# Kernel tuning notes

Measured on AMD Instinct MI355X. Metric: run time of the kernel, lower is better.

## Reference

```python
import jax, jax.numpy as jnp
import numpy as np

B, N, P = 8192, 4096, 8
D = N // P  # 512
EPS = 1e-5


def setup_inputs() -> dict:
    key = jax.random.key(0)
    ks = jax.random.split(key, 7)
    bound = 1.0 / np.sqrt(D)
    return {
        "x": jax.random.normal(ks[0], (B, N), dtype=jnp.float32),
        "weights1": jax.random.normal(ks[1], (P, D, D), dtype=jnp.float32) * bound,
        "bias1": jax.random.uniform(ks[2], (N,), jnp.float32, -bound, bound),
        "weights2": jax.random.normal(ks[3], (P, D, D), dtype=jnp.float32) * bound,
        "bias2": jax.random.uniform(ks[4], (N,), jnp.float32, -bound, bound),
        "bn_weight": jnp.ones((N,), jnp.float32),
        "bn_bias": jnp.zeros((N,), jnp.float32),
        "gamma3": jax.random.normal(ks[5], (N,), jnp.float32) * 0.1,
        "beta3": jax.random.normal(ks[6], (N,), jnp.float32) * 0.1,
    }


def _block_matmul(x, w):
    # x: [B, N], w: [P, D, D] -> equivalent to x @ block_diag(*w)
    b = x.shape[0]
    return jnp.einsum("bpd,pde->bpe", x.reshape(b, P, D), w).reshape(b, N)


def reference(x, weights1, bias1, weights2, bias2, bn_weight, bn_bias, gamma3, beta3):
    h = _block_matmul(x, weights1) + bias1  # [B, N]
    # BatchNorm1d in training mode: biased batch statistics over the batch axis
    mean = jnp.mean(h, axis=0)
    var = jnp.mean((h - mean) ** 2, axis=0)
    o1 = (h - mean) * jax.lax.rsqrt(var + EPS) * bn_weight + bn_bias
    o3 = _block_matmul(o1, weights2) + bias2 + x  # residual
    # sigmoid-gated activation: (gamma + sigmoid(beta*x)*(1-gamma)) * x
    o4 = (gamma3 + jax.nn.sigmoid(beta3 * o3) * (1.0 - gamma3)) * o3
    return o4
```

## Files before the change

### kernel.cpp

```cpp
#include <hip/hip_runtime.h>
#include <hip/hip_bf16.h>
#include <cstdint>
#include <cstddef>

#define B_ROWS 8192
#define N_COLS 4096
#define P_BLK 8
#define D_BLK 512
#define EPSV 1e-5f

typedef __bf16 bf16x8 __attribute__((ext_vector_type(8)));
typedef float f32x4 __attribute__((ext_vector_type(4)));

__device__ __forceinline__ void async_ld16(const void* g, void* l) {
    __builtin_amdgcn_global_load_lds(
        (const __attribute__((address_space(1))) void*)g,
        (__attribute__((address_space(3))) void*)l,
        16, 0, 0);
}

__device__ __forceinline__ void decode_tile(int n, int& row_base, int& col_base) {
    const int row_tile = n >> 5;
    const int col_tile = ((n & 7) << 2) | ((n >> 3) & 3);
    row_base = row_tile * 128;
    col_base = col_tile * 128;
}

__global__ __launch_bounds__(256) void cvt_x_k(const float* __restrict__ x,
                                               __hip_bfloat16* __restrict__ xb) {
    size_t i = ((size_t)blockIdx.x * 256 + threadIdx.x) * 8;
    float4 v0 = *(const float4*)(x + i);
    float4 v1 = *(const float4*)(x + i + 4);
    union { __hip_bfloat16 h[8]; uint4 u; } r;
    r.h[0] = __float2bfloat16(v0.x); r.h[1] = __float2bfloat16(v0.y);
    r.h[2] = __float2bfloat16(v0.z); r.h[3] = __float2bfloat16(v0.w);
    r.h[4] = __float2bfloat16(v1.x); r.h[5] = __float2bfloat16(v1.y);
    r.h[6] = __float2bfloat16(v1.z); r.h[7] = __float2bfloat16(v1.w);
    *(uint4*)(xb + i) = r.u;
}

__global__ __launch_bounds__(256) void tr_w_k(const float* __restrict__ W,
                                              const float* __restrict__ scale,
                                              __hip_bfloat16* __restrict__ Wt) {
    __shared__ float t[32][33];
    int p = blockIdx.z;
    int d0 = blockIdx.x * 32, e0 = blockIdx.y * 32;
    const float* Wp = W + (size_t)p * D_BLK * D_BLK;
    for (int j = 0; j < 32; j += 8) {
        int d = d0 + threadIdx.y + j;
        float v = Wp[(size_t)d * D_BLK + e0 + threadIdx.x];
        if (scale) v *= scale[p * D_BLK + d];
        t[threadIdx.y + j][threadIdx.x] = v;
    }
    __syncthreads();
    __hip_bfloat16* Wtp = Wt + (size_t)p * D_BLK * D_BLK;
    for (int j = 0; j < 32; j += 8) {
        int e = e0 + threadIdx.y + j;
        Wtp[(size_t)e * D_BLK + d0 + threadIdx.x] =
            __float2bfloat16(t[threadIdx.x][threadIdx.y + j]);
    }
}

__global__ __launch_bounds__(256) void finalize_k(const float* __restrict__ sum,
                                                  const float* __restrict__ sumsq,
                                                  const float* __restrict__ bnw,
                                                  const float* __restrict__ bnb,
                                                  float* __restrict__ a,
                                                  float* __restrict__ c) {
    int i = blockIdx.x * 256 + threadIdx.x;
    float m = sum[i] * (1.0f / B_ROWS);
    float var = sumsq[i] * (1.0f / B_ROWS) - m * m;
    float ai = bnw[i] * rsqrtf(var + EPSV);
    a[i] = ai;
    c[i] = bnb[i] - m * ai;
}

__global__ __launch_bounds__(256) void bias2p_k(const float* __restrict__ W2,
                                                const float* __restrict__ c,
                                                const float* __restrict__ bias2,
                                                float* __restrict__ out) {
    int col = blockIdx.x * 256 + threadIdx.x;
    int p = col >> 9;
    int e = col & (D_BLK - 1);
    int d0 = blockIdx.y * (D_BLK / 8);
    const float* Wp = W2 + (size_t)p * D_BLK * D_BLK + (size_t)d0 * D_BLK + e;
    const float* cp = c + p * D_BLK + d0;
    float acc = (blockIdx.y == 0) ? bias2[col] : 0.0f;
    for (int d = 0; d < D_BLK / 8; d++) acc += cp[d] * Wp[(size_t)d * D_BLK];
    atomicAdd(&out[col], acc);
}

__device__ __forceinline__ void gemm_core(const __hip_bfloat16* __restrict__ A,
                                          const __hip_bfloat16* __restrict__ Bt,
                                          int row_base, int col_base,
                                          f32x4 acc[4][4]) {
    __shared__ __hip_bfloat16 As[2][128 * 32];
    __shared__ __hip_bfloat16 Bs[2][128 * 32];

    const int tid = threadIdx.x;
    const int lane = tid & 63;
    const int wave = tid >> 6;
    const int wm = (wave >> 1) * 64;
    const int wn = (wave & 1) * 64;
    const int p = col_base >> 9;
    const int ebase = col_base & (D_BLK - 1);

    const int ar = tid >> 2;
    const int c4 = tid & 3;
    const int kq8 = (c4 ^ ((tid >> 3) & 3)) * 8;
    const int dst_off = ar * 32 + c4 * 8;

    const __hip_bfloat16* a_src0 = A + (size_t)(row_base + ar) * N_COLS + p * D_BLK + kq8;
    const __hip_bfloat16* a_src1 = a_src0 + (size_t)64 * N_COLS;
    const __hip_bfloat16* b_src0 = Bt + (size_t)(p * D_BLK + ebase + ar) * D_BLK + kq8;
    const __hip_bfloat16* b_src1 = b_src0 + (size_t)64 * D_BLK;

    const int fm = lane & 15;
    const int fkoff = ((lane >> 4) ^ ((fm >> 1) & 3)) * 8;

    for (int i = 0; i < 4; i++)
        for (int j = 0; j < 4; j++)
            acc[i][j] = (f32x4){0.0f, 0.0f, 0.0f, 0.0f};

    async_ld16(a_src0, &As[0][dst_off]);
    async_ld16(a_src1, &As[0][dst_off + 64 * 32]);
    async_ld16(b_src0, &Bs[0][dst_off]);
    async_ld16(b_src1, &Bs[0][dst_off + 64 * 32]);

    int cur = 0;
    for (int k0 = 0; k0 < D_BLK; k0 += 32) {
        if (k0 + 32 < D_BLK) {
            __hip_bfloat16* ad = &As[cur ^ 1][dst_off];
            __hip_bfloat16* bd = &Bs[cur ^ 1][dst_off];
            async_ld16(a_src0 + 32, ad);
            async_ld16(a_src1 + 32, ad + 64 * 32);
            async_ld16(b_src0 + 32, bd);
            async_ld16(b_src1 + 32, bd + 64 * 32);
            a_src0 += 32; a_src1 += 32; b_src0 += 32; b_src1 += 32;
            asm volatile("s_waitcnt vmcnt(4)" ::: "memory");
        } else {
            asm volatile("s_waitcnt vmcnt(0)" ::: "memory");
        }
        __builtin_amdgcn_s_barrier();
        asm volatile("" ::: "memory");

        bf16x8 af[4], bfr[4];
        const __hip_bfloat16* Asc = &As[cur][0];
        const __hip_bfloat16* Bsc = &Bs[cur][0];
#pragma unroll
        for (int i = 0; i < 4; i++)
            af[i] = *(const bf16x8*)&Asc[(wm + i * 16 + fm) * 32 + fkoff];
#pragma unroll
        for (int j = 0; j < 4; j++)
            bfr[j] = *(const bf16x8*)&Bsc[(wn + j * 16 + fm) * 32 + fkoff];
        asm volatile("s_waitcnt lgkmcnt(0)" ::: "memory");
        __builtin_amdgcn_sched_barrier(0);
        __builtin_amdgcn_s_barrier();
        asm volatile("" ::: "memory");

#pragma unroll
        for (int i = 0; i < 4; i++)
#pragma unroll
            for (int j = 0; j < 4; j++)
                acc[i][j] = __builtin_amdgcn_mfma_f32_16x16x32_bf16(
                    af[i], bfr[j], acc[i][j], 0, 0, 0);
        cur ^= 1;
    }
}

__global__ __launch_bounds__(256) void gemm1_k(const __hip_bfloat16* __restrict__ xb,
                                               const __hip_bfloat16* __restrict__ w1t,
                                               const float* __restrict__ bias1,
                                               __hip_bfloat16* __restrict__ h,
                                               float* __restrict__ sum,
                                               float* __restrict__ sumsq) {
    int row_base, col_base;
    decode_tile(blockIdx.x, row_base, col_base);

    f32x4 acc[4][4];
    gemm_core(xb, w1t, row_base, col_base, acc);

    const int tid = threadIdx.x;
    const int lane = tid & 63;
    const int wave = tid >> 6;
    const int wm = (wave >> 1) * 64;
    const int wn = (wave & 1) * 64;
    const int cr = (lane >> 4) * 4;
    const int cc = lane & 15;

#pragma unroll
    for (int j = 0; j < 4; j++) {
        const int col = col_base + wn + j * 16 + cc;
        const float b1 = bias1[col];
        float s = 0.0f, sq = 0.0f;
#pragma unroll
        for (int i = 0; i < 4; i++) {
            const int row0 = row_base + wm + i * 16 + cr;
#pragma unroll
            for (int r = 0; r < 4; r++) {
                float v = acc[i][j][r] + b1;
                h[(size_t)(row0 + r) * N_COLS + col] = __float2bfloat16(v);
                s += v;
                sq += v * v;
            }
        }
        s  += __shfl_xor(s, 16);  s  += __shfl_xor(s, 32);
        sq += __shfl_xor(sq, 16); sq += __shfl_xor(sq, 32);
        if (lane < 16) {
            atomicAdd(&sum[col], s);
            atomicAdd(&sumsq[col], sq);
        }
    }
}

__global__ __launch_bounds__(256) void gemm2_k(const __hip_bfloat16* __restrict__ h,
                                               const __hip_bfloat16* __restrict__ w2t,
                                               const float* __restrict__ bias2p,
                                               const __hip_bfloat16* __restrict__ xb,
                                               const float* __restrict__ gamma3,
                                               const float* __restrict__ beta3,
                                               float* __restrict__ out) {
    int row_base, col_base;
    decode_tile(blockIdx.x, row_base, col_base);

    f32x4 acc[4][4];
    gemm_core(h, w2t, row_base, col_base, acc);

    const int tid = threadIdx.x;
    const int lane = tid & 63;
    const int wave = tid >> 6;
    const int wm = (wave >> 1) * 64;
    const int wn = (wave & 1) * 64;
    const int cr = (lane >> 4) * 4;
    const int cc = lane & 15;

#pragma unroll
    for (int j = 0; j < 4; j++) {
        const int col = col_base + wn + j * 16 + cc;
        const float bb = bias2p[col];
        const float g  = gamma3[col];
        const float be = beta3[col];
#pragma unroll
        for (int i = 0; i < 4; i++) {
            const int row0 = row_base + wm + i * 16 + cr;
#pragma unroll
            for (int r = 0; r < 4; r++) {
                const size_t idx = (size_t)(row0 + r) * N_COLS + col;
                float o3 = acc[i][j][r] + bb + __bfloat162float(xb[idx]);
                float sg = __fdividef(1.0f, 1.0f + __expf(-be * o3));
                out[idx] = (g + sg * (1.0f - g)) * o3;
            }
        }
    }
}

extern "C" void kernel_launch(void* const* d_in, const int* in_sizes, int n_in,
                              void* d_out, int out_size, void* d_ws, size_t ws_size,
                              hipStream_t stream) {
    const float* x     = (const float*)d_in[0];
    const float* W1    = (const float*)d_in[1];
    const float* bias1 = (const float*)d_in[2];
    const float* W2    = (const float*)d_in[3];
    const float* bias2 = (const float*)d_in[4];
    const float* bnw   = (const float*)d_in[5];
    const float* bnb   = (const float*)d_in[6];
    const float* gam3  = (const float*)d_in[7];
    const float* bet3  = (const float*)d_in[8];
    float* out = (float*)d_out;

    char* ws = (char*)d_ws;
    const size_t XB_BYTES = (size_t)B_ROWS * N_COLS * 2;
    const size_t H_BYTES  = (size_t)B_ROWS * N_COLS * 2;
    const size_t WT_BYTES = (size_t)P_BLK * D_BLK * D_BLK * 2;
    const size_t V_BYTES  = (size_t)N_COLS * 4;

    __hip_bfloat16* xb   = (__hip_bfloat16*)(ws);
    __hip_bfloat16* hbuf = (__hip_bfloat16*)(ws + XB_BYTES);
    __hip_bfloat16* w1t  = (__hip_bfloat16*)(ws + XB_BYTES + H_BYTES);
    __hip_bfloat16* w2t  = (__hip_bfloat16*)(ws + XB_BYTES + H_BYTES + WT_BYTES);
    float* sums  = (float*)(ws + XB_BYTES + H_BYTES + 2 * WT_BYTES);
    float* sumsq = sums + N_COLS;
    float* b2p   = sums + 2 * N_COLS;
    float* a_sc  = sums + 3 * N_COLS;
    float* c_sh  = sums + 4 * N_COLS;

    (void)in_sizes; (void)n_in; (void)out_size; (void)ws_size;

    hipMemsetAsync(sums, 0, 3 * V_BYTES, stream);

    cvt_x_k<<<dim3((B_ROWS * N_COLS) / (256 * 8)), dim3(256), 0, stream>>>(x, xb);
    tr_w_k<<<dim3(16, 16, 8), dim3(32, 8), 0, stream>>>(W1, nullptr, w1t);
    gemm1_k<<<dim3((B_ROWS / 128) * (N_COLS / 128)), dim3(256), 0, stream>>>(
        xb, w1t, bias1, hbuf, sums, sumsq);
    finalize_k<<<dim3(N_COLS / 256), dim3(256), 0, stream>>>(sums, sumsq, bnw, bnb, a_sc, c_sh);
    tr_w_k<<<dim3(16, 16, 8), dim3(32, 8), 0, stream>>>(W2, a_sc, w2t);
    bias2p_k<<<dim3(N_COLS / 256, 8), dim3(256), 0, stream>>>(W2, c_sh, bias2, b2p);
    gemm2_k<<<dim3((B_ROWS / 128) * (N_COLS / 128)), dim3(256), 0, stream>>>(
        hbuf, w2t, b2p, xb, gam3, bet3, out);
}
```

Baseline: 390.5 us.

## Use 256x256 GEMM tiles with 8-wave ping-pong schedule and fuse prep kernels

Replaces the 128x128, 4-wave double-buffered GEMM core with a 256x256 tile. It uses 512 threads, 128KB of dynamic LDS, an XOR-swizzled layout, and an interleaved phase schedule that issues staged async loads between MFMA groups with s_setprio. The intent is more data reuse per LDS load and better overlap of global loads with matrix work. Separately, it fuses the x conversion with the W1 transpose, and folds the BN finalize into the W2 transpose and bias-projection kernels, which cuts the launch count. The risks are the large LDS footprint and higher register pressure limiting occupancy, plus fewer blocks for load balancing.

Result: slower. 425.1 us (+8.9%).

```diff
diff --git a/kernel.cpp b/kernel.cpp
--- a/kernel.cpp
+++ b/kernel.cpp
@@ -19,172 +19,319 @@
         16, 0, 0);
 }
 
-__device__ __forceinline__ void decode_tile(int n, int& row_base, int& col_base) {
-    const int row_tile = n >> 5;
-    const int col_tile = ((n & 7) << 2) | ((n >> 3) & 3);
-    row_base = row_tile * 128;
-    col_base = col_tile * 128;
-}
-
-__global__ __launch_bounds__(256) void cvt_x_k(const float* __restrict__ x,
-                                               __hip_bfloat16* __restrict__ xb) {
-    size_t i = ((size_t)blockIdx.x * 256 + threadIdx.x) * 8;
-    float4 v0 = *(const float4*)(x + i);
-    float4 v1 = *(const float4*)(x + i + 4);
-    union { __hip_bfloat16 h[8]; uint4 u; } r;
-    r.h[0] = __float2bfloat16(v0.x); r.h[1] = __float2bfloat16(v0.y);
-    r.h[2] = __float2bfloat16(v0.z); r.h[3] = __float2bfloat16(v0.w);
-    r.h[4] = __float2bfloat16(v1.x); r.h[5] = __float2bfloat16(v1.y);
-    r.h[6] = __float2bfloat16(v1.z); r.h[7] = __float2bfloat16(v1.w);
-    *(uint4*)(xb + i) = r.u;
-}
-
-__global__ __launch_bounds__(256) void tr_w_k(const float* __restrict__ W,
-                                              const float* __restrict__ scale,
-                                              __hip_bfloat16* __restrict__ Wt) {
-    __shared__ float t[32][33];
-    int p = blockIdx.z;
-    int d0 = blockIdx.x * 32, e0 = blockIdx.y * 32;
-    const float* Wp = W + (size_t)p * D_BLK * D_BLK;
+__global__ __launch_bounds__(256) void prep_k(const float* __restrict__ x,
+                                              __hip_bfloat16* __restrict__ xb,
+                                              const float* __restrict__ W1,
+                                              __hip_bfloat16* __restrict__ w1t) {
+    __shared__ float tl[32][33];
+    if (blockIdx.x < 16384) {
+        size_t i = ((size_t)blockIdx.x * 256 + threadIdx.x) * 8;
+        float4 v0 = *(const float4*)(x + i);
+        float4 v1 = *(const float4*)(x + i + 4);
+        union { __hip_bfloat16 h[8]; uint4 u; } r;
+        r.h[0] = __float2bfloat16(v0.x); r.h[1] = __float2bfloat16(v0.y);
+        r.h[2] = __float2bfloat16(v0.z); r.h[3] = __float2bfloat16(v0.w);
+        r.h[4] = __float2bfloat16(v1.x); r.h[5] = __float2bfloat16(v1.y);
+        r.h[6] = __float2bfloat16(v1.z); r.h[7] = __float2bfloat16(v1.w);
+        *(uint4*)(xb + i) = r.u;
+        return;
+    }
+    const int n = blockIdx.x - 16384;
+    const int p = n >> 8;
+    const int rem = n & 255;
+    const int d0 = (rem & 15) * 32, e0 = (rem >> 4) * 32;
+    const int tx = threadIdx.x & 31, ty = threadIdx.x >> 5;
+    const float* Wp = W1 + (size_t)p * D_BLK * D_BLK;
     for (int j = 0; j < 32; j += 8) {
-        int d = d0 + threadIdx.y + j;
-        float v = Wp[(size_t)d * D_BLK + e0 + threadIdx.x];
-        if (scale) v *= scale[p * D_BLK + d];
-        t[threadIdx.y + j][threadIdx.x] = v;
+        int d = d0 + ty + j;
+        tl[ty + j][tx] = Wp[(size_t)d * D_BLK + e0 + tx];
     }
     __syncthreads();
-    __hip_bfloat16* Wtp = Wt + (size_t)p * D_BLK * D_BLK;
+    __hip_bfloat16* Wtp = w1t + (size_t)p * D_BLK * D_BLK;
     for (int j = 0; j < 32; j += 8) {
-        int e = e0 + threadIdx.y + j;
-        Wtp[(size_t)e * D_BLK + d0 + threadIdx.x] =
-            __float2bfloat16(t[threadIdx.x][threadIdx.y + j]);
-    }
-}
-
-__global__ __launch_bounds__(256) void finalize_k(const float* __restrict__ sum,
-                                                  const float* __restrict__ sumsq,
-                                                  const float* __restrict__ bnw,
-                                                  const float* __restrict__ bnb,
-                                                  float* __restrict__ a,
-                                                  float* __restrict__ c) {
-    int i = blockIdx.x * 256 + threadIdx.x;
-    float m = sum[i] * (1.0f / B_ROWS);
-    float var = sumsq[i] * (1.0f / B_ROWS) - m * m;
-    float ai = bnw[i] * rsqrtf(var + EPSV);
-    a[i] = ai;
-    c[i] = bnb[i] - m * ai;
-}
-
-__global__ __launch_bounds__(256) void bias2p_k(const float* __restrict__ W2,
-                                                const float* __restrict__ c,
-                                                const float* __restrict__ bias2,
-                                                float* __restrict__ out) {
-    int col = blockIdx.x * 256 + threadIdx.x;
-    int p = col >> 9;
-    int e = col & (D_BLK - 1);
-    int d0 = blockIdx.y * (D_BLK / 8);
-    const float* Wp = W2 + (size_t)p * D_BLK * D_BLK + (size_t)d0 * D_BLK + e;
-    const float* cp = c + p * D_BLK + d0;
-    float acc = (blockIdx.y == 0) ? bias2[col] : 0.0f;
-    for (int d = 0; d < D_BLK / 8; d++) acc += cp[d] * Wp[(size_t)d * D_BLK];
-    atomicAdd(&out[col], acc);
-}
-
-__device__ __forceinline__ void gemm_core(const __hip_bfloat16* __restrict__ A,
-                                          const __hip_bfloat16* __restrict__ Bt,
-                                          int row_base, int col_base,
-                                          f32x4 acc[4][4]) {
-    __shared__ __hip_bfloat16 As[2][128 * 32];
-    __shared__ __hip_bfloat16 Bs[2][128 * 32];
+        int e = e0 + ty + j;
+        Wtp[(size_t)e * D_BLK + d0 + tx] = __float2bfloat16(tl[tx][ty + j]);
+    }
+}
+
+__global__ __launch_bounds__(256) void mid_k(const float* __restrict__ W2,
+                                             const float* __restrict__ sums,
+                                             const float* __restrict__ sumsq,
+                                             const float* __restrict__ bnw,
+                                             const float* __restrict__ bnb,
+                                             const float* __restrict__ bias2,
+                                             __hip_bfloat16* __restrict__ w2t,
+                                             float* __restrict__ b2p) {
+    __shared__ float tl[32][33];
+    __shared__ float as_[32];
+    const float invB = 1.0f / B_ROWS;
+    if (blockIdx.x < 2048) {
+        const int n = blockIdx.x;
+        const int p = n >> 8;
+        const int rem = n & 255;
+        const int d0 = (rem & 15) * 32, e0 = (rem >> 4) * 32;
+        const int tx = threadIdx.x & 31, ty = threadIdx.x >> 5;
+        if (threadIdx.x < 32) {
+            int idx = p * D_BLK + d0 + threadIdx.x;
+            float m = sums[idx] * invB;
+            float var = sumsq[idx] * invB - m * m;
+            as_[threadIdx.x] = bnw[idx] * rsqrtf(var + EPSV);
+        }
+        __syncthreads();
+        const float* Wp = W2 + (size_t)p * D_BLK * D_BLK;
+        for (int j = 0; j < 32; j += 8) {
+            int d = d0 + ty + j;
+            tl[ty + j][tx] = Wp[(size_t)d * D_BLK + e0 + tx] * as_[ty + j];
+        }
+        __syncthreads();
+        __hip_bfloat16* Wtp = w2t + (size_t)p * D_BLK * D_BLK;
+        for (int j = 0; j < 32; j += 8) {
+            int e = e0 + ty + j;
+            Wtp[(size_t)e * D_BLK + d0 + tx] = __float2bfloat16(tl[tx][ty + j]);
+        }
+        return;
+    }
+    const int n2 = blockIdx.x - 2048;
+    const int colblk = n2 & 15, chunk = n2 >> 4;
+    const int col = colblk * 256 + threadIdx.x;
+    const int p = col >> 9;
+    const int e = col & (D_BLK - 1);
+    const int d0 = chunk * 64;
+    float acc = (chunk == 0) ? bias2[col] : 0.0f;
+    for (int d = 0; d < 64; d++) {
+        int idx = p * D_BLK + d0 + d;
+        float m = sums[idx] * invB;
+        float var = sumsq[idx] * invB - m * m;
+        float ai = bnw[idx] * rsqrtf(var + EPSV);
+        float ci = bnb[idx] - m * ai;
+        acc += ci * W2[((size_t)p * D_BLK + d0 + d) * D_BLK + e];
+    }
+    atomicAdd(&b2p[col], acc);
+}
+
+__device__ __forceinline__ void gemm_core256(const __hip_bfloat16* __restrict__ A,
+                                             const __hip_bfloat16* __restrict__ Bt,
+                                             int row_base, int col_base,
+                                             f32x4 acc[8][4]) {
+    extern __shared__ __align__(16) __hip_bfloat16 lds[];
+    __hip_bfloat16* ldsA = lds;
+    __hip_bfloat16* ldsB = lds + 32768;
 
     const int tid = threadIdx.x;
     const int lane = tid & 63;
-    const int wave = tid >> 6;
-    const int wm = (wave >> 1) * 64;
-    const int wn = (wave & 1) * 64;
+    const int w = tid >> 6;
     const int p = col_base >> 9;
     const int ebase = col_base & (D_BLK - 1);
 
-    const int ar = tid >> 2;
-    const int c4 = tid & 3;
-    const int kq8 = (c4 ^ ((tid >> 3) & 3)) * 8;
-    const int dst_off = ar * 32 + c4 * 8;
-
-    const __hip_bfloat16* a_src0 = A + (size_t)(row_base + ar) * N_COLS + p * D_BLK + kq8;
-    const __hip_bfloat16* a_src1 = a_src0 + (size_t)64 * N_COLS;
-    const __hip_bfloat16* b_src0 = Bt + (size_t)(p * D_BLK + ebase + ar) * D_BLK + kq8;
-    const __hip_bfloat16* b_src1 = b_src0 + (size_t)64 * D_BLK;
+    const int r1 = tid >> 3;
+    const int ce = ((((tid >> 3) ^ tid) & 7) << 3);
+    const __hip_bfloat16* aBase = A + (size_t)(row_base + r1) * N_COLS + p * D_BLK + ce;
+    const __hip_bfloat16* bBase = Bt + (size_t)(p * D_BLK + ebase + r1) * D_BLK + ce;
+    __hip_bfloat16* dA = ldsA + tid * 8;
+    __hip_bfloat16* dB = ldsB + tid * 8;
+
+#define STAGE_A(buf, half, kt) do { \
+        const __hip_bfloat16* g_ = aBase + (size_t)(half) * 128 * N_COLS + (kt) * 64; \
+        __hip_bfloat16* d_ = dA + ((buf) * 2 + (half)) * 8192; \
+        async_ld16(g_, d_); \
+        async_ld16(g_ + (size_t)64 * N_COLS, d_ + 4096); } while (0)
+#define STAGE_B(buf, half, kt) do { \
+        const __hip_bfloat16* g_ = bBase + (size_t)(half) * 128 * D_BLK + (kt) * 64; \
+        __hip_bfloat16* d_ = dB + ((buf) * 2 + (half)) * 8192; \
+        async_ld16(g_, d_); \
+        async_ld16(g_ + (size_t)64 * D_BLK, d_ + 4096); } while (0)
 
     const int fm = lane & 15;
-    const int fkoff = ((lane >> 4) ^ ((fm >> 1) & 3)) * 8;
-
-    for (int i = 0; i < 4; i++)
+    const int kq = lane >> 4;
+    const int f0 = ((kq * 16) ^ ((fm & 7) << 4)) >> 1;
+    const int f1 = ((64 + kq * 16) ^ ((fm & 7) << 4)) >> 1;
+    const int ha = w >> 2;
+    const int hb = (w >> 1) & 1;
+    const int lcb = (w & 1) * 64;
+
+#define LDA(buf, i, kk) (*(const bf16x8*)(ldsA + (buf) * 16384 + ha * 8192 + \
+        (((i) * 16 + fm) * 64) + ((kk) ? f1 : f0)))
+#define LDB(buf, j, kk) (*(const bf16x8*)(ldsB + (buf) * 16384 + hb * 8192 + \
+        ((lcb + (j) * 16 + fm) * 64) + ((kk) ? f1 : f0)))
+
+#define PHASE_TOP() do { __builtin_amdgcn_s_barrier(); \
+        asm volatile("s_waitcnt lgkmcnt(0)" ::: "memory"); \
+        __builtin_amdgcn_sched_barrier(0); \
+        __builtin_amdgcn_s_setprio(1); } while (0)
+#define PHASE_BOT() do { __builtin_amdgcn_s_setprio(0); \
+        __builtin_amdgcn_s_barrier(); \
+        asm volatile("" ::: "memory"); } while (0)
+
+#pragma unroll
+    for (int i = 0; i < 8; i++)
+#pragma unroll
         for (int j = 0; j < 4; j++)
             acc[i][j] = (f32x4){0.0f, 0.0f, 0.0f, 0.0f};
 
-    async_ld16(a_src0, &As[0][dst_off]);
-    async_ld16(a_src1, &As[0][dst_off + 64 * 32]);
-    async_ld16(b_src0, &Bs[0][dst_off]);
-    async_ld16(b_src1, &Bs[0][dst_off + 64 * 32]);
-
-    int cur = 0;
-    for (int k0 = 0; k0 < D_BLK; k0 += 32) {
-        if (k0 + 32 < D_BLK) {
-            __hip_bfloat16* ad = &As[cur ^ 1][dst_off];
-            __hip_bfloat16* bd = &Bs[cur ^ 1][dst_off];
-            async_ld16(a_src0 + 32, ad);
-            async_ld16(a_src1 + 32, ad + 64 * 32);
-            async_ld16(b_src0 + 32, bd);
-            async_ld16(b_src1 + 32, bd + 64 * 32);
-            a_src0 += 32; a_src1 += 32; b_src0 += 32; b_src1 += 32;
+    STAGE_B(0, 0, 0); STAGE_A(0, 0, 0); STAGE_B(0, 1, 0); STAGE_A(0, 1, 0);
+    STAGE_B(1, 0, 1); STAGE_A(1, 0, 1);
+    asm volatile("s_waitcnt vmcnt(4)" ::: "memory");
+    __builtin_amdgcn_s_barrier();
+    asm volatile("" ::: "memory");
+
+#pragma unroll
+    for (int it = 0; it < 4; ++it) {
+        const int kO = 2 * it + 1, kE2 = 2 * it + 2, kO2 = 2 * it + 3;
+        const bool last = (it == 3);
+        bf16x8 ar[4][2], b0[2][2], b1[2][2];
+
+#pragma unroll
+        for (int i = 0; i < 4; i++) { ar[i][0] = LDA(0, i, 0); ar[i][1] = LDA(0, i, 1); }
+#pragma unroll
+        for (int j = 0; j < 2; j++) { b0[j][0] = LDB(0, j, 0); b0[j][1] = LDB(0, j, 1); }
+        STAGE_B(1, 1, kO);
+        PHASE_TOP();
+#pragma unroll
+        for (int i = 0; i < 4; i++)
+#pragma unroll
+            for (int j = 0; j < 2; j++)
+#pragma unroll
+                for (int kk = 0; kk < 2; kk++)
+                    acc[i][j] = __builtin_amdgcn_mfma_f32_16x16x32_bf16(
+                        ar[i][kk], b0[j][kk], acc[i][j], 0, 0, 0);
+        PHASE_BOT();
+
+#pragma unroll
+        for (int j = 0; j < 2; j++) { b1[j][0] = LDB(0, j + 2, 0); b1[j][1] = LDB(0, j + 2, 1); }
+        STAGE_A(1, 1, kO);
+        PHASE_TOP();
+#pragma unroll
+        for (int i = 0; i < 4; i++)
+#pragma unroll
+            for (int j = 0; j < 2; j++)
+#pragma unroll
+                for (int kk = 0; kk < 2; kk++)
+                    acc[i][j + 2] = __builtin_amdgcn_mfma_f32_16x16x32_bf16(
+                        ar[i][kk], b1[j][kk], acc[i][j + 2], 0, 0, 0);
+        PHASE_BOT();
+
+#pragma unroll
+        for (int i = 0; i < 4; i++) { ar[i][0] = LDA(0, i + 4, 0); ar[i][1] = LDA(0, i + 4, 1); }
+        if (!last) STAGE_B(0, 0, kE2);
+        PHASE_TOP();
+#pragma unroll
+        for (int i = 0; i < 4; i++)
+#pragma unroll
+            for (int j = 0; j < 2; j++)
+#pragma unroll
+                for (int kk = 0; kk < 2; kk++)
+                    acc[i + 4][j + 2] = __builtin_amdgcn_mfma_f32_16x16x32_bf16(
+                        ar[i][kk], b1[j][kk], acc[i + 4][j + 2], 0, 0, 0);
+        PHASE_BOT();
+
+        if (!last) {
+            STAGE_A(0, 0, kE2);
             asm volatile("s_waitcnt vmcnt(4)" ::: "memory");
         } else {
             asm volatile("s_waitcnt vmcnt(0)" ::: "memory");
         }
-        __builtin_amdgcn_s_barrier();
-        asm volatile("" ::: "memory");
-
-        bf16x8 af[4], bfr[4];
-        const __hip_bfloat16* Asc = &As[cur][0];
-        const __hip_bfloat16* Bsc = &Bs[cur][0];
-#pragma unroll
-        for (int i = 0; i < 4; i++)
-            af[i] = *(const bf16x8*)&Asc[(wm + i * 16 + fm) * 32 + fkoff];
-#pragma unroll
-        for (int j = 0; j < 4; j++)
-            bfr[j] = *(const bf16x8*)&Bsc[(wn + j * 16 + fm) * 32 + fkoff];
-        asm volatile("s_waitcnt lgkmcnt(0)" ::: "memory");
-        __builtin_amdgcn_sched_barrier(0);
-        __builtin_amdgcn_s_barrier();
-        asm volatile("" ::: "memory");
-
-#pragma unroll
-        for (int i = 0; i < 4; i++)
-#pragma unroll
-            for (int j = 0; j < 4; j++)
-                acc[i][j] = __builtin_amdgcn_mfma_f32_16x16x32_bf16(
-                    af[i], bfr[j], acc[i][j], 0, 0, 0);
-        cur ^= 1;
-    }
-}
-
-__global__ __launch_bounds__(256) void gemm1_k(const __hip_bfloat16* __restrict__ xb,
-                                               const __hip_bfloat16* __restrict__ w1t,
-                                               const float* __restrict__ bias1,
-                                               __hip_bfloat16* __restrict__ h,
-                                               float* __restrict__ sum,
-                                               float* __restrict__ sumsq) {
+        PHASE_TOP();
+#pragma unroll
+        for (int i = 0; i < 4; i++)
+#pragma unroll
+            for (int j = 0; j < 2; j++)
+#pragma unroll
+                for (int kk = 0; kk < 2; kk++)
+                    acc[i + 4][j] = __builtin_amdgcn_mfma_f32_16x16x32_bf16(
+                        ar[i][kk], b0[j][kk], acc[i + 4][j], 0, 0, 0);
+        PHASE_BOT();
+
+#pragma unroll
+        for (int i = 0; i < 4; i++) { ar[i][0] = LDA(1, i, 0); ar[i][1] = LDA(1, i, 1); }
+#pragma unroll
+        for (int j = 0; j < 2; j++) { b0[j][0] = LDB(1, j, 0); b0[j][1] = LDB(1, j, 1); }
+        if (!last) STAGE_B(0, 1, kE2);
+        PHASE_TOP();
+#pragma unroll
+        for (int i = 0; i < 4; i++)
+#pragma unroll
+            for (int j = 0; j < 2; j++)
+#pragma unroll
+                for (int kk = 0; kk < 2; kk++)
+                    acc[i][j] = __builtin_amdgcn_mfma_f32_16x16x32_bf16(
+                        ar[i][kk], b0[j][kk], acc[i][j], 0, 0, 0);
+        PHASE_BOT();
+
+#pragma unroll
+        for (int j = 0; j < 2; j++) { b1[j][0] = LDB(1, j + 2, 0); b1[j][1] = LDB(1, j + 2, 1); }
+        if (!last) STAGE_A(0, 1, kE2);
+        PHASE_TOP();
+#pragma unroll
+        for (int i = 0; i < 4; i++)
+#pragma unroll
+            for (int j = 0; j < 2; j++)
+#pragma unroll
+                for (int kk = 0; kk < 2; kk++)
+                    acc[i][j + 2] = __builtin_amdgcn_mfma_f32_16x16x32_bf16(
+                        ar[i][kk], b1[j][kk], acc[i][j + 2], 0, 0, 0);
+        PHASE_BOT();
+
+#pragma unroll
+        for (int i = 0; i < 4; i++) { ar[i][0] = LDA(1, i + 4, 0); ar[i][1] = LDA(1, i + 4, 1); }
+        if (!last) STAGE_B(1, 0, kO2);
+        PHASE_TOP();
+#pragma unroll
+        for (int i = 0; i < 4; i++)
+#pragma unroll
+            for (int j = 0; j < 2; j++)
+#pragma unroll
+                for (int kk = 0; kk < 2; kk++)
+                    acc[i + 4][j + 2] = __builtin_amdgcn_mfma_f32_16x16x32_bf16(
+                        ar[i][kk], b1[j][kk], acc[i + 4][j + 2], 0, 0, 0);
+        PHASE_BOT();
+
+        if (!last) {
+            STAGE_A(1, 0, kO2);
+            asm volatile("s_waitcnt vmcnt(4)" ::: "memory");
+        }
+        PHASE_TOP();
+#pragma unroll
+        for (int i = 0; i < 4; i++)
+#pragma unroll
+            for (int j = 0; j < 2; j++)
+#pragma unroll
+                for (int kk = 0; kk < 2; kk++)
+                    acc[i + 4][j] = __builtin_amdgcn_mfma_f32_16x16x32_bf16(
+                        ar[i][kk], b0[j][kk], acc[i + 4][j], 0, 0, 0);
+        PHASE_BOT();
+    }
+#undef STAGE_A
+#undef STAGE_B
+#undef LDA
+#undef LDB
+#undef PHASE_TOP
+#undef PHASE_BOT
+}
+
+__device__ __forceinline__ void decode_tile256(int n, int& row_base, int& col_base) {
+    const int p = n & 7;
+    const int m = n >> 3;
+    row_base = (m >> 1) * 256;
+    col_base = (((p << 1) | (m & 1))) * 256;
+}
+
+__global__ __launch_bounds__(512, 2) void gemm1_k(const __hip_bfloat16* __restrict__ xb,
+                                                  const __hip_bfloat16* __restrict__ w1t,
+                                                  const float* __restrict__ bias1,
+                                                  __hip_bfloat16* __restrict__ h,
+                                                  float* __restrict__ sum,
+                                                  float* __restrict__ sumsq) {
     int row_base, col_base;
-    decode_tile(blockIdx.x, row_base, col_base);
-
-    f32x4 acc[4][4];
-    gemm_core(xb, w1t, row_base, col_base, acc);
+    decode_tile256(blockIdx.x, row_base, col_base);
+
+    f32x4 acc[8][4];
+    gemm_core256(xb, w1t, row_base, col_base, acc);
 
     const int tid = threadIdx.x;
     const int lane = tid & 63;
-    const int wave = tid >> 6;
-    const int wm = (wave >> 1) * 64;
-    const int wn = (wave & 1) * 64;
+    const int w = tid >> 6;
+    const int wm = (w >> 2) * 128;
+    const int wn = (w & 3) * 64;
     const int cr = (lane >> 4) * 4;
     const int cc = lane & 15;
 
@@ -194,7 +341,7 @@
         const float b1 = bias1[col];
         float s = 0.0f, sq = 0.0f;
 #pragma unroll
-        for (int i = 0; i < 4; i++) {
+        for (int i = 0; i < 8; i++) {
             const int row0 = row_base + wm + i * 16 + cr;
 #pragma unroll
             for (int r = 0; r < 4; r++) {
@@ -213,24 +360,24 @@
     }
 }
 
-__global__ __launch_bounds__(256) void gemm2_k(const __hip_bfloat16* __restrict__ h,
-                                               const __hip_bfloat16* __restrict__ w2t,
-                                               const float* __restrict__ bias2p,
-                                               const __hip_bfloat16* __restrict__ xb,
-                                               const float* __restrict__ gamma3,
-                                               const float* __restrict__ beta3,
-                                               float* __restrict__ out) {
+__global__ __launch_bounds__(512, 2) void gemm2_k(const __hip_bfloat16* __restrict__ h,
+                                                  const __hip_bfloat16* __restrict__ w2t,
+                                                  const float* __restrict__ bias2p,
+                                                  const __hip_bfloat16* __restrict__ xb,
+                                                  const float* __restrict__ gamma3,
+                                                  const float* __restrict__ beta3,
+                                                  float* __restrict__ out) {
     int row_base, col_base;
-    decode_tile(blockIdx.x, row_base, col_base);
-
-    f32x4 acc[4][4];
-    gemm_core(h, w2t, row_base, col_base, acc);
+    decode_tile256(blockIdx.x, row_base, col_base);
+
+    f32x4 acc[8][4];
+    gemm_core256(h, w2t, row_base, col_base, acc);
 
     const int tid = threadIdx.x;
     const int lane = tid & 63;
-    const int wave = tid >> 6;
-    const int wm = (wave >> 1) * 64;
-    const int wn = (wave & 1) * 64;
+    const int w = tid >> 6;
+    const int wm = (w >> 2) * 128;
+    const int wn = (w & 3) * 64;
     const int cr = (lane >> 4) * 4;
     const int cc = lane & 15;
 
@@ -241,7 +388,7 @@
         const float g  = gamma3[col];
         const float be = beta3[col];
 #pragma unroll
-        for (int i = 0; i < 4; i++) {
+        for (int i = 0; i < 8; i++) {
             const int row0 = row_base + wm + i * 16 + cr;
 #pragma unroll
             for (int r = 0; r < 4; r++) {
@@ -281,20 +428,25 @@
     float* sums  = (float*)(ws + XB_BYTES + H_BYTES + 2 * WT_BYTES);
     float* sumsq = sums + N_COLS;
     float* b2p   = sums + 2 * N_COLS;
-    float* a_sc  = sums + 3 * N_COLS;
-    float* c_sh  = sums + 4 * N_COLS;
 
     (void)in_sizes; (void)n_in; (void)out_size; (void)ws_size;
 
+    static int attr_set = 0;
+    if (!attr_set) {
+        hipFuncSetAttribute((const void*)gemm1_k,
+                            hipFuncAttributeMaxDynamicSharedMemorySize, 131072);
+        hipFuncSetAttribute((const void*)gemm2_k,
+                            hipFuncAttributeMaxDynamicSharedMemorySize, 131072);
+        attr_set = 1;
+    }
+
     hipMemsetAsync(sums, 0, 3 * V_BYTES, stream);
 
-    cvt_x_k<<<dim3((B_ROWS * N_COLS) / (256 * 8)), dim3(256), 0, stream>>>(x, xb);
-    tr_w_k<<<dim3(16, 16, 8), dim3(32, 8), 0, stream>>>(W1, nullptr, w1t);
-    gemm1_k<<<dim3((B_ROWS / 128) * (N_COLS / 128)), dim3(256), 0, stream>>>(
+    prep_k<<<dim3(16384 + 2048), dim3(256), 0, stream>>>(x, xb, W1, w1t);
+    gemm1_k<<<dim3((B_ROWS / 256) * (N_COLS / 256)), dim3(512), 131072, stream>>>(
         xb, w1t, bias1, hbuf, sums, sumsq);
-    finalize_k<<<dim3(N_COLS / 256), dim3(256), 0, stream>>>(sums, sumsq, bnw, bnb, a_sc, c_sh);
-    tr_w_k<<<dim3(16, 16, 8), dim3(32, 8), 0, stream>>>(W2, a_sc, w2t);
-    bias2p_k<<<dim3(N_COLS / 256, 8), dim3(256), 0, stream>>>(W2, c_sh, bias2, b2p);
-    gemm2_k<<<dim3((B_ROWS / 128) * (N_COLS / 128)), dim3(256), 0, stream>>>(
+    mid_k<<<dim3(2048 + 128), dim3(256), 0, stream>>>(
+        W2, sums, sumsq, bnw, bnb, bias2, w2t, b2p);
+    gemm2_k<<<dim3((B_ROWS / 256) * (N_COLS / 256)), dim3(512), 131072, stream>>>(
         hbuf, w2t, b2p, xb, gam3, bet3, out);
 }
```
